# Kernel optimization log

Hardware: AMD Instinct MI355X
Metric: run time of the kernel (lower is better)

## Reference

```python
import jax, jax.numpy as jnp
import numpy as np

S, IN, H, D, B, BOT, IMG, TXT = 4, 4096, 2048, 6, 1024, 128, 768, 768


def _gelu(x):
    # torch nn.GELU default = exact erf gelu
    return jax.nn.gelu(x, approximate=False)


def _ln(x, g, b, eps=1e-5):
    mu = jnp.mean(x, axis=-1, keepdims=True)
    var = jnp.mean(jnp.square(x - mu), axis=-1, keepdims=True)
    return g * (x - mu) / jnp.sqrt(var + eps) + b


def setup_inputs() -> dict:
    key = jax.random.key(0)
    ks = jax.random.split(key, 16)
    n = lambda k, shp, s=0.02: jax.random.normal(k, shp, dtype=jnp.float32) * s
    return dict(
        voxels=jax.random.normal(ks[0], (B, IN), dtype=jnp.float32),
        subject_ids=jax.random.randint(ks[1], (B,), 0, S, dtype=jnp.int32),
        # per-subject encoder params, stacked on leading subject axis S
        ad_down_w=n(ks[2], (S, IN, BOT)), ad_down_b=n(ks[3], (S, BOT)),
        ad_up_w=n(ks[4], (S, BOT, IN)), ad_up_b=n(ks[5], (S, IN)),
        enc_w=n(ks[6], (S, IN, H)), enc_b=n(ks[7], (S, H)),
        enc_ln_g=jnp.ones((S, H), jnp.float32), enc_ln_b=jnp.zeros((S, H), jnp.float32),
        # shared ResidualStack params, stacked on leading depth axis D
        bb_w=n(ks[8], (D, H, H)), bb_b=n(ks[9], (D, H)),
        bb_ln_g=jnp.ones((D, H), jnp.float32), bb_ln_b=jnp.zeros((D, H), jnp.float32),
        # heads
        img_w=n(ks[10], (H, IMG)), img_b=n(ks[11], (IMG,)),
        txt_w=n(ks[12], (H, TXT)), txt_b=n(ks[13], (TXT,)),
    )


def _forward(voxels, subject_ids, ad_down_w, ad_down_b, ad_up_w, ad_up_b,
             enc_w, enc_b, enc_ln_g, enc_ln_b, bb_w, bb_b, bb_ln_g, bb_ln_b,
             img_w, img_b, txt_w, txt_b):
    # --- subject-routed encoders (dense dispatch over the small fixed subject set) ---
    def enc_one(dw, db, uw, ub, ew, eb, g, be):
        # BottleneckAdapter: x + up(gelu(down(x)))
        h = voxels + _gelu(voxels @ dw + db) @ uw + ub          # [B, IN]
        # Linear -> LayerNorm -> GELU (Dropout is identity in eval)
        return _gelu(_ln(h @ ew + eb, g, be))                    # [B, H]

    feats_all = jax.vmap(enc_one)(ad_down_w, ad_down_b, ad_up_w, ad_up_b,
                                  enc_w, enc_b, enc_ln_g, enc_ln_b)  # [S, B, H]
    x = feats_all[subject_ids, jnp.arange(voxels.shape[0])]          # [B, H] pick own subject

    # --- shared ResidualStack: x = x + gelu(ln(linear(x))) per block ---
    def step(x, p):
        w, b, g, be = p
        return x + _gelu(_ln(x @ w + b, g, be)), None

    x, _ = jax.lax.scan(step, x, (bb_w, bb_b, bb_ln_g, bb_ln_b))

    return x @ img_w + img_b, x @ txt_w + txt_b  # (image_embedding, text_embedding)


def reference(voxels, subject_ids, ad_down_w, ad_down_b, ad_up_w, ad_up_b,
              enc_w, enc_b, enc_ln_g, enc_ln_b, bb_w, bb_b, bb_ln_g, bb_ln_b,
              img_w, img_b, txt_w, txt_b):
    return _forward(voxels, subject_ids, ad_down_w, ad_down_b, ad_up_w, ad_up_b,
                    enc_w, enc_b, enc_ln_g, enc_ln_b, bb_w, bb_b, bb_ln_g, bb_ln_b,
                    img_w, img_b, txt_w, txt_b)
```

## Files before the change

kernel.cpp:

```cpp
#include <hip/hip_runtime.h>
#include <hip/hip_bf16.h>
#include <stdint.h>

typedef __bf16 bf16x8 __attribute__((ext_vector_type(8)));
typedef float  f32x4  __attribute__((ext_vector_type(4)));
typedef float  vf4    __attribute__((ext_vector_type(4)));

#define DEV __device__ __forceinline__

constexpr int SUBJ  = 4;
constexpr int IN    = 4096;
constexpr int H     = 2048;
constexpr int DEPTH = 6;
constexpr int BATCH = 1024;
constexpr int BOT   = 128;
constexpr int IMG   = 768;
constexpr int TXT   = 768;
constexpr int MP    = 1408;
constexpr int MT    = 11;

DEV float gelu_exact(float x){ return 0.5f*x*(1.0f + erff(x*0.70710678118654752440f)); }

DEV uint16_t bf16_bits(float x){
  __hip_bfloat16 h = __float2bfloat16(x);
  return *reinterpret_cast<uint16_t*>(&h);
}
DEV float bfu(uint32_t w, int hi){
  uint32_t x = hi ? (w & 0xffff0000u) : (w << 16);
  return __uint_as_float(x);
}
DEV float bf2f(uint16_t u){ uint32_t x = (uint32_t)u << 16; return __uint_as_float(x); }

struct CvtSeg { const float* src; size_t dst_off; };
struct CvtParams { CvtSeg s[6]; size_t total_items; };

__global__ void convert_weights(CvtParams p, __hip_bfloat16* __restrict__ dst){
  size_t it = (size_t)blockIdx.x*blockDim.x + threadIdx.x;
  if (it >= p.total_items) return;
  size_t e = it << 4;
  int si = 0;
  #pragma unroll
  for (int i = 1; i < 6; ++i) if (e >= p.s[i].dst_off) si = i;
  const float* s = p.s[si].src + (e - p.s[si].dst_off);
  float4 a = *reinterpret_cast<const float4*>(s);
  float4 b = *reinterpret_cast<const float4*>(s + 4);
  float4 c = *reinterpret_cast<const float4*>(s + 8);
  float4 d = *reinterpret_cast<const float4*>(s + 12);
  uint16_t o[16] = {bf16_bits(a.x), bf16_bits(a.y), bf16_bits(a.z), bf16_bits(a.w),
                    bf16_bits(b.x), bf16_bits(b.y), bf16_bits(b.z), bf16_bits(b.w),
                    bf16_bits(c.x), bf16_bits(c.y), bf16_bits(c.z), bf16_bits(c.w),
                    bf16_bits(d.x), bf16_bits(d.y), bf16_bits(d.z), bf16_bits(d.w)};
  *reinterpret_cast<uint4*>(dst + e)     = *reinterpret_cast<const uint4*>(&o[0]);
  *reinterpret_cast<uint4*>(dst + e + 8) = *reinterpret_cast<const uint4*>(&o[8]);
}

__global__ void sort_kernel(const int* __restrict__ ids, int* __restrict__ rowmap,
                            int* __restrict__ tileS){
  __shared__ int hist[16][4];
  __shared__ int basew[16][4];
  __shared__ int pstart[5];
  int tid = threadIdx.x;
  if (tid < MP) rowmap[tid] = -1;
  if (tid + 1024 < MP) rowmap[tid + 1024] = -1;
  int w = tid >> 6, lane = tid & 63;
  int my = ids[tid];
  unsigned long long mymask = 0ull;
  #pragma unroll
  for (int s = 0; s < 4; ++s){
    unsigned long long m = __ballot(my == s);
    if (lane == 0) hist[w][s] = (int)__popcll(m);
    if (s == my) mymask = m;
  }
  int myrank = (int)__popcll(mymask & ((1ull << lane) - 1ull));
  __syncthreads();
  if (tid == 0){
    for (int s = 0; s < 4; ++s){
      int run = 0;
      for (int ww = 0; ww < 16; ++ww){ basew[ww][s] = run; run += hist[ww][s]; }
      hist[0][s] = run;
    }
    pstart[0] = 0;
    for (int s = 0; s < 4; ++s) pstart[s+1] = pstart[s] + ((hist[0][s] + 127) & ~127);
  }
  __syncthreads();
  int pos = pstart[my] + basew[w][my] + myrank;
  rowmap[pos] = tid;
  if (tid < MT){
    int row0 = tid << 7, s = -1;
    for (int ss = 0; ss < 4; ++ss) if (row0 >= pstart[ss] && row0 < pstart[ss+1]) s = ss;
    tileS[tid] = s;
  }
}

__global__ void gather_voxels(const float* __restrict__ vox, const int* __restrict__ rowmap,
                              __hip_bfloat16* __restrict__ Vs){
  int r = blockIdx.x, tid = threadIdx.x;
  int orig = rowmap[r];
  #pragma unroll
  for (int i = 0; i < 4; ++i){
    int c = (i*256 + tid) << 2;
    float4 v = {0.f,0.f,0.f,0.f};
    if (orig >= 0) v = *reinterpret_cast<const float4*>(vox + (size_t)orig*IN + c);
    __hip_bfloat16 o[4] = {__float2bfloat16(v.x), __float2bfloat16(v.y),
                           __float2bfloat16(v.z), __float2bfloat16(v.w)};
    *reinterpret_cast<uint2*>(Vs + (size_t)r*IN + c) = *reinterpret_cast<const uint2*>(o);
  }
}

enum { EPI_SPLIT = 0, EPI_RES_BF16 = 1, EPI_HEADS = 3 };

template<int EPI, int TAG>
__global__ __launch_bounds__(256, 2)
void gemm_bf16(const __hip_bfloat16* __restrict__ A, int lda,
               const __hip_bfloat16* __restrict__ Bw, int ldn, long long wsub,
               const int* __restrict__ tileS, const int* __restrict__ rowmap,
               int nx, int qnt, int ksplit,
               const float* __restrict__ bias, int biassub,
               const float* __restrict__ resid, int ldres,
               __hip_bfloat16* __restrict__ outb, int ldo,
               size_t pstride, const __hip_bfloat16* __restrict__ Bw2)
{
  int b   = blockIdx.x;
  int xcd = b & 7;
  int r0  = b >> 3;
  int mt  = r0 % MT;
  int q   = r0 / MT;
  int kzi = xcd / nx + (q / qnt) * (8 / nx);
  int nt  = (q % qnt) * nx + (xcd % nx);

  int s = tileS[mt];
  if (s < 0) return;
  const __hip_bfloat16* Ab = A + (size_t)mt*128*lda;

  const __hip_bfloat16* Bb;
  int ntl = nt;
  if constexpr (EPI == EPI_HEADS){
    if (nt < 6){ Bb = Bw  + (size_t)nt*128; }
    else       { Bb = Bw2 + (size_t)(nt-6)*128; }
    ntl = nt;
  } else {
    Bb = Bw + (size_t)s*wsub + (size_t)nt*128;
  }

  int kb = kzi * ksplit;
  int nk = ksplit >> 6;

  __shared__ __hip_bfloat16 sA[2][128*64];
  __shared__ __hip_bfloat16 sB[2][128*64];

  int tid = threadIdx.x;
  int lane = tid & 63;
  int wv = tid >> 6, wr = wv >> 1, wc = wv & 1;

  int kq = tid >> 5;
  int nq = tid & 31;
  int n4 = nq << 2;

  f32x4 acc[4][4];
  #pragma unroll
  for (int i = 0; i < 4; ++i)
    #pragma unroll
    for (int j = 0; j < 4; ++j) acc[i][j] = (f32x4){0.f,0.f,0.f,0.f};

  auto stageA = [&](int buf, int k0){
    #pragma unroll
    for (int i = 0; i < 4; ++i){
      int cell = i*256 + tid;
      int row = cell >> 3, cc = cell & 7;
      int kg = k0 + ((cc ^ (row & 7)) << 3);
      __builtin_amdgcn_global_load_lds(
        (const __attribute__((address_space(1))) void*)(Ab + (size_t)row*lda + kg),
        (__attribute__((address_space(3))) void*)(&sA[buf][cell<<3]), 16, 0, 0);
    }
  };

  auto stageB_load = [&](int k0g, uint2* F){
    const __hip_bfloat16* p = Bb + (size_t)(k0g + (kq<<3))*ldn + n4;
    #pragma unroll
    for (int rr = 0; rr < 8; ++rr)
      F[rr] = *reinterpret_cast<const uint2*>(p + (size_t)rr*ldn);
  };
  auto stageB_write = [&](int buf, const uint2* F){
    #pragma unroll
    for (int j = 0; j < 4; ++j){
      int n = n4 + j;
      int cell = (kq ^ (n >> 3) ^ n) & 7;
      auto US = [&](int rr)->uint32_t{
        return (((const uint32_t*)&F[rr])[j >> 1] >> ((j & 1) * 16)) & 0xffffu;
      };
      uint4 d;
      d.x = US(0) | (US(1) << 16);
      d.y = US(2) | (US(3) << 16);
      d.z = US(4) | (US(5) << 16);
      d.w = US(6) | (US(7) << 16);
      *reinterpret_cast<uint4*>(&sB[buf][(n<<6) + (cell<<3)]) = d;
    }
  };

  uint2 F[8];
  stageB_load(kb, F);
  stageA(0, kb);
  stageB_write(0, F);
  __syncthreads();

  for (int t = 0; t < nk; ++t){
    if (t+1 < nk){
      stageB_load(kb + ((t+1)<<6), F);
      stageA((t+1)&1, kb + ((t+1)<<6));
    }
    const char* baseA = (const char*)(&sA[t&1][0]);
    const char* baseB = (const char*)(&sB[t&1][0]);
    int rA = (wr<<6) + (lane & 15);
    int rB = (wc<<6) + (lane & 15);
    #pragma unroll
    for (int kk = 0; kk < 2; ++kk){
      int koffA = ((((kk<<5) + ((lane>>4)<<3)) << 1)) ^ ((lane & 7) << 4);
      bf16x8 av[4], bv[4];
      #pragma unroll
      for (int f = 0; f < 4; ++f){
        int rowA = rA + f*16;
        av[f] = *reinterpret_cast<const bf16x8*>(baseA + (size_t)rowA*128 + koffA);
        int rowB = rB + f*16;
        int cellB = (((kk<<2) + (lane>>4)) ^ (rowB >> 3) ^ rowB) & 7;
        bv[f] = *reinterpret_cast<const bf16x8*>(baseB + (size_t)rowB*128 + (cellB<<4));
      }
      #pragma unroll
      for (int i = 0; i < 4; ++i)
        #pragma unroll
        for (int j = 0; j < 4; ++j)
          acc[i][j] = __builtin_amdgcn_mfma_f32_16x16x32_bf16(av[i], bv[j], acc[i][j], 0, 0, 0);
    }
    if (t+1 < nk) stageB_write((t+1)&1, F);
    __syncthreads();
  }

  #pragma unroll
  for (int i = 0; i < 4; ++i){
    int rbase = (mt<<7) + (wr<<6) + (i<<4) + ((lane>>4)<<2);
    #pragma unroll
    for (int j = 0; j < 4; ++j){
      int colp = (wc<<6) + (j<<4) + (lane & 15);
      #pragma unroll
      for (int qq = 0; qq < 4; ++qq){
        int r = rbase + qq;
        float v = acc[i][j][qq];
        if constexpr (EPI == EPI_SPLIT){
          int col = (nt<<7) + colp;
          outb[(size_t)kzi*pstride + (size_t)r*ldo + col] = __float2bfloat16(v);
        } else if constexpr (EPI == EPI_RES_BF16){
          int col = (nt<<7) + colp;
          int orig = rowmap[r];
          if (orig >= 0){
            v += bias[(size_t)s*biassub + col] + resid[(size_t)orig*ldres + col];
            outb[(size_t)r*ldo + col] = __float2bfloat16(v);
          }
        } else {
          int col = (ntl<<7) + colp;
          outb[(size_t)kzi*pstride + (size_t)r*ldo + col] = __float2bfloat16(v);
        }
      }
    }
  }
}

template<int NPART>
__global__ void t1_epilogue(const __hip_bfloat16* __restrict__ Tp, const float* __restrict__ db,
                            const int* __restrict__ rowmap, const int* __restrict__ tileS,
                            __hip_bfloat16* __restrict__ T1){
  int idx = blockIdx.x*256 + threadIdx.x;
  int r = idx >> 7, c = idx & 127;
  float v = 0.f;
  if (rowmap[r] >= 0){
    int s = tileS[r >> 7];
    float acc = 0.f;
    #pragma unroll
    for (int p = 0; p < NPART; ++p)
      acc += bf2f(*reinterpret_cast<const uint16_t*>(Tp + (size_t)p*MP*BOT + idx));
    v = gelu_exact(acc + db[s*BOT + c]);
  }
  T1[idx] = __float2bfloat16(v);
}

template<int RES, int NPART>
__global__ void ln_gelu_kernel(const __hip_bfloat16* __restrict__ Zp, size_t pstride,
                               const float* __restrict__ g,
                               const float* __restrict__ b, int gsub,
                               const float* __restrict__ lb,
                               const int* __restrict__ tileS, const int* __restrict__ rowmap,
                               __hip_bfloat16* __restrict__ Xb){
  int r = blockIdx.x, tid = threadIdx.x;
  size_t rowoff = (size_t)r * H;
  int c0 = tid << 3;
  int orig = rowmap[r];
  if (orig < 0){
    uint4 zu = {0u,0u,0u,0u};
    *reinterpret_cast<uint4*>(Xb + rowoff + c0) = zu;
    return;
  }
  int si = gsub ? tileS[r>>7] : 0;
  const float* gp  = g  + (size_t)si*gsub;
  const float* bp  = b  + (size_t)si*gsub;
  const float* lbp = lb + (size_t)si*gsub;
  float z[8];
  #pragma unroll
  for (int j = 0; j < 8; ++j) z[j] = lbp[c0+j];
  #pragma unroll
  for (int p = 0; p < NPART; ++p){
    uint4 v = *reinterpret_cast<const uint4*>(Zp + p*pstride + rowoff + c0);
    z[0] += bfu(v.x,0); z[1] += bfu(v.x,1);
    z[2] += bfu(v.y,0); z[3] += bfu(v.y,1);
    z[4] += bfu(v.z,0); z[5] += bfu(v.z,1);
    z[6] += bfu(v.w,0); z[7] += bfu(v.w,1);
  }
  float s1 = 0.f, s2 = 0.f;
  #pragma unroll
  for (int j = 0; j < 8; ++j){ s1 += z[j]; s2 += z[j]*z[j]; }
  #pragma unroll
  for (int m = 32; m >= 1; m >>= 1){ s1 += __shfl_xor(s1, m); s2 += __shfl_xor(s2, m); }
  __shared__ float red[4][2];
  int wv = tid >> 6, lane = tid & 63;
  if (lane == 0){ red[wv][0] = s1; red[wv][1] = s2; }
  __syncthreads();
  s1 = red[0][0]+red[1][0]+red[2][0]+red[3][0];
  s2 = red[0][1]+red[1][1]+red[2][1]+red[3][1];
  const float invH = 1.f / (float)H;
  float mu  = s1 * invH;
  float var = s2 * invH - mu*mu;
  float rs  = rsqrtf(var + 1e-5f);
  float o[8];
  #pragma unroll
  for (int j = 0; j < 8; ++j){
    float t = (z[j]-mu)*rs*gp[c0+j] + bp[c0+j];
    o[j] = gelu_exact(t);
  }
  if constexpr (RES){
    uint4 xv = *reinterpret_cast<const uint4*>(Xb + rowoff + c0);
    o[0] += bfu(xv.x,0); o[1] += bfu(xv.x,1);
    o[2] += bfu(xv.y,0); o[3] += bfu(xv.y,1);
    o[4] += bfu(xv.z,0); o[5] += bfu(xv.z,1);
    o[6] += bfu(xv.w,0); o[7] += bfu(xv.w,1);
  }
  __hip_bfloat16 ob[8];
  #pragma unroll
  for (int j = 0; j < 8; ++j) ob[j] = __float2bfloat16(o[j]);
  *reinterpret_cast<uint4*>(Xb + rowoff + c0) = *reinterpret_cast<const uint4*>(ob);
}

template<int NPART>
__global__ void head_combine(const __hip_bfloat16* __restrict__ Hp, size_t pstride,
                             const float* __restrict__ img_b, const float* __restrict__ txt_b,
                             const int* __restrict__ rowmap,
                             float* __restrict__ oimg, float* __restrict__ otxt){
  int r = blockIdx.x;
  int orig = rowmap[r];
  if (orig < 0) return;
  int col = threadIdx.x << 2;
  size_t base = (size_t)r*(IMG+TXT) + col;
  float4 acc = {0.f,0.f,0.f,0.f};
  #pragma unroll
  for (int p = 0; p < NPART; ++p){
    uint2 u = *reinterpret_cast<const uint2*>(Hp + (size_t)p*pstride + base);
    acc.x += bfu(u.x,0); acc.y += bfu(u.x,1);
    acc.z += bfu(u.y,0); acc.w += bfu(u.y,1);
  }
  float4 bb = (col < IMG)
            ? *reinterpret_cast<const float4*>(img_b + col)
            : *reinterpret_cast<const float4*>(txt_b + (col - IMG));
  float4 o = {acc.x+bb.x, acc.y+bb.y, acc.z+bb.z, acc.w+bb.w};
  if (col < IMG) *reinterpret_cast<float4*>(oimg + (size_t)orig*IMG + col) = o;
  else           *reinterpret_cast<float4*>(otxt + (size_t)orig*TXT + (col-IMG)) = o;
}

extern "C" void kernel_launch(void* const* d_in, const int* in_sizes, int n_in,
                              void* d_out, int out_size, void* d_ws, size_t ws_size,
                              hipStream_t stream){
  (void)in_sizes; (void)n_in; (void)out_size; (void)ws_size;
  const float* vox       = (const float*)d_in[0];
  const int*   ids       = (const int*)  d_in[1];
  const float* ad_down_w = (const float*)d_in[2];
  const float* ad_down_b = (const float*)d_in[3];
  const float* ad_up_w   = (const float*)d_in[4];
  const float* ad_up_b   = (const float*)d_in[5];
  const float* enc_w     = (const float*)d_in[6];
  const float* enc_b     = (const float*)d_in[7];
  const float* enc_ln_g  = (const float*)d_in[8];
  const float* enc_ln_bb = (const float*)d_in[9];
  const float* bb_w      = (const float*)d_in[10];
  const float* bb_b      = (const float*)d_in[11];
  const float* bb_ln_g   = (const float*)d_in[12];
  const float* bb_ln_b   = (const float*)d_in[13];
  const float* img_w     = (const float*)d_in[14];
  const float* img_b     = (const float*)d_in[15];
  const float* txt_w     = (const float*)d_in[16];
  const float* txt_b     = (const float*)d_in[17];
  float* out = (float*)d_out;

  const size_t N_DOWN = (size_t)SUBJ*IN*BOT;
  const size_t N_UP   = (size_t)SUBJ*BOT*IN;
  const size_t N_ENC  = (size_t)SUBJ*IN*H;
  const size_t N_BB   = (size_t)DEPTH*H*H;
  const size_t N_IMG  = (size_t)H*IMG;
  const size_t N_TXT  = (size_t)H*TXT;

  char* wp = (char*)d_ws;
  auto alloc = [&](size_t bytes)->char*{ char* p = wp; wp += (bytes + 255) & ~(size_t)255; return p; };
  int* rowmap = (int*)alloc(MP * sizeof(int));
  int* tileS  = (int*)alloc(MT * sizeof(int));
  __hip_bfloat16* Wbf = (__hip_bfloat16*)alloc((N_DOWN+N_UP+N_ENC+N_BB+N_IMG+N_TXT)*2);
  __hip_bfloat16* w_down = Wbf;
  __hip_bfloat16* w_up   = w_down + N_DOWN;
  __hip_bfloat16* w_enc  = w_up   + N_UP;
  __hip_bfloat16* w_bb   = w_enc  + N_ENC;
  __hip_bfloat16* w_img  = w_bb   + N_BB;
  __hip_bfloat16* w_txt  = w_img  + N_IMG;
  __hip_bfloat16* Vs    = (__hip_bfloat16*)alloc((size_t)MP*IN*2);
  __hip_bfloat16* T1p   = (__hip_bfloat16*)alloc((size_t)32*MP*BOT*2);
  __hip_bfloat16* T1    = (__hip_bfloat16*)alloc((size_t)MP*BOT*2);
  __hip_bfloat16* Hs    = (__hip_bfloat16*)alloc((size_t)MP*IN*2);
  __hip_bfloat16* Zp    = (__hip_bfloat16*)alloc((size_t)4*MP*H*2);
  __hip_bfloat16* Hp    = Zp;
  __hip_bfloat16* Xb    = (__hip_bfloat16*)alloc((size_t)MP*H*2);

  const size_t ZPS = (size_t)MP*H;
  const size_t TPS = (size_t)MP*BOT;
  const size_t HPS = (size_t)MP*(IMG+TXT);

  CvtParams cp;
  size_t off = 0;
  cp.s[0] = {ad_down_w, off}; off += N_DOWN;
  cp.s[1] = {ad_up_w,   off}; off += N_UP;
  cp.s[2] = {enc_w,     off}; off += N_ENC;
  cp.s[3] = {bb_w,      off}; off += N_BB;
  cp.s[4] = {img_w,     off}; off += N_IMG;
  cp.s[5] = {txt_w,     off}; off += N_TXT;
  cp.total_items = off >> 4;
  int cvt_blocks = (int)((cp.total_items + 255) / 256);
  convert_weights<<<cvt_blocks, 256, 0, stream>>>(cp, Wbf);

  sort_kernel<<<1, 1024, 0, stream>>>(ids, rowmap, tileS);
  gather_voxels<<<MP, 256, 0, stream>>>(vox, rowmap, Vs);

  gemm_bf16<EPI_SPLIT,1><<<MT*32, 256, 0, stream>>>(
      Vs, IN, w_down, BOT, (long long)IN*BOT, tileS, rowmap, 1, 1, 128,
      nullptr, 0, nullptr, 0, T1p, BOT, TPS, nullptr);
  t1_epilogue<32><<<MP*BOT/256, 256, 0, stream>>>(T1p, ad_down_b, rowmap, tileS, T1);

  gemm_bf16<EPI_RES_BF16,2><<<MT*32, 256, 0, stream>>>(
      T1, BOT, w_up, IN, (long long)BOT*IN, tileS, rowmap, 8, 4, 128,
      ad_up_b, IN, vox, IN, Hs, IN, 0, nullptr);

  gemm_bf16<EPI_SPLIT,3><<<MT*8*8, 256, 0, stream>>>(
      Hs, IN, w_enc, H, (long long)IN*H, tileS, rowmap, 2, 8, 1024,
      nullptr, 0, nullptr, 0, Zp, H, ZPS, nullptr);
  ln_gelu_kernel<0,4><<<MP, 256, 0, stream>>>(Zp, ZPS, enc_ln_g, enc_ln_bb, H, enc_b,
                                              tileS, rowmap, Xb);

  for (int d = 0; d < DEPTH; ++d){
    gemm_bf16<EPI_SPLIT,4><<<MT*4*8, 256, 0, stream>>>(
        Xb, H, w_bb + (size_t)d*H*H, H, 0, tileS, rowmap, 4, 4, 1024,
        nullptr, 0, nullptr, 0, Zp, H, ZPS, nullptr);
    ln_gelu_kernel<1,2><<<MP, 256, 0, stream>>>(Zp, ZPS, bb_ln_g + (size_t)d*H,
                                                bb_ln_b + (size_t)d*H, 0, bb_b + (size_t)d*H,
                                                tileS, rowmap, Xb);
  }

  gemm_bf16<EPI_HEADS,5><<<MT*3*8, 256, 0, stream>>>(
      Xb, H, w_img, IMG, 0, tileS, rowmap, 4, 3, 1024,
      nullptr, 0, nullptr, 0, Hp, IMG+TXT, HPS, w_txt);
  head_combine<2><<<MP, 384, 0, stream>>>(Hp, HPS, img_b, txt_b, rowmap,
                                          out, out + (size_t)BATCH*IMG);
}
```

Measured before the change: 433.4 us.

## Overlap weight bf16 conversion with preceding GEMMs via extra tail blocks

The single up-front weight conversion kernel is split up. Each weight tensor is now converted by extra blocks appended to the grid of the GEMM that runs just before that weight is first needed, so conversion overlaps with GEMM work. Only the adapter-down weights are still converted by a standalone kernel. This removes a serial memory-bound pass at the start. The cost is extra blocks competing with GEMM blocks for CUs and bandwidth, plus a larger kernel signature.

```diff
diff --git a/kernel.cpp b/kernel.cpp
--- a/kernel.cpp
+++ b/kernel.cpp
@@ -4,7 +4,6 @@
 
 typedef __bf16 bf16x8 __attribute__((ext_vector_type(8)));
 typedef float  f32x4  __attribute__((ext_vector_type(4)));
-typedef float  vf4    __attribute__((ext_vector_type(4)));
 
 #define DEV __device__ __forceinline__
 
@@ -31,27 +30,24 @@
 }
 DEV float bf2f(uint16_t u){ uint32_t x = (uint32_t)u << 16; return __uint_as_float(x); }
 
-struct CvtSeg { const float* src; size_t dst_off; };
-struct CvtParams { CvtSeg s[6]; size_t total_items; };
-
-__global__ void convert_weights(CvtParams p, __hip_bfloat16* __restrict__ dst){
-  size_t it = (size_t)blockIdx.x*blockDim.x + threadIdx.x;
-  if (it >= p.total_items) return;
-  size_t e = it << 4;
-  int si = 0;
-  #pragma unroll
-  for (int i = 1; i < 6; ++i) if (e >= p.s[i].dst_off) si = i;
-  const float* s = p.s[si].src + (e - p.s[si].dst_off);
+DEV void cvt16(const float* __restrict__ s, __hip_bfloat16* __restrict__ d){
   float4 a = *reinterpret_cast<const float4*>(s);
   float4 b = *reinterpret_cast<const float4*>(s + 4);
   float4 c = *reinterpret_cast<const float4*>(s + 8);
-  float4 d = *reinterpret_cast<const float4*>(s + 12);
+  float4 e = *reinterpret_cast<const float4*>(s + 12);
   uint16_t o[16] = {bf16_bits(a.x), bf16_bits(a.y), bf16_bits(a.z), bf16_bits(a.w),
                     bf16_bits(b.x), bf16_bits(b.y), bf16_bits(b.z), bf16_bits(b.w),
                     bf16_bits(c.x), bf16_bits(c.y), bf16_bits(c.z), bf16_bits(c.w),
-                    bf16_bits(d.x), bf16_bits(d.y), bf16_bits(d.z), bf16_bits(d.w)};
-  *reinterpret_cast<uint4*>(dst + e)     = *reinterpret_cast<const uint4*>(&o[0]);
-  *reinterpret_cast<uint4*>(dst + e + 8) = *reinterpret_cast<const uint4*>(&o[8]);
+                    bf16_bits(e.x), bf16_bits(e.y), bf16_bits(e.z), bf16_bits(e.w)};
+  *reinterpret_cast<uint4*>(d)     = *reinterpret_cast<const uint4*>(&o[0]);
+  *reinterpret_cast<uint4*>(d + 8) = *reinterpret_cast<const uint4*>(&o[8]);
+}
+
+__global__ void convert_plain(const float* __restrict__ src, __hip_bfloat16* __restrict__ dst,
+                              size_t items){
+  size_t it = (size_t)blockIdx.x*blockDim.x + threadIdx.x;
+  if (it >= items) return;
+  cvt16(src + (it<<4), dst + (it<<4));
 }
 
 __global__ void sort_kernel(const int* __restrict__ ids, int* __restrict__ rowmap,
@@ -118,9 +114,16 @@
                const float* __restrict__ bias, int biassub,
                const float* __restrict__ resid, int ldres,
                __hip_bfloat16* __restrict__ outb, int ldo,
-               size_t pstride, const __hip_bfloat16* __restrict__ Bw2)
+               size_t pstride, const __hip_bfloat16* __restrict__ Bw2,
+               int ggrid, const float* __restrict__ csrc,
+               __hip_bfloat16* __restrict__ cdst, size_t citems)
 {
-  int b   = blockIdx.x;
+  int b = blockIdx.x;
+  if (b >= ggrid){
+    size_t it = (size_t)(b - ggrid)*blockDim.x + threadIdx.x;
+    if (it < citems) cvt16(csrc + (it<<4), cdst + (it<<4));
+    return;
+  }
   int xcd = b & 7;
   int r0  = b >> 3;
   int mt  = r0 % MT;
@@ -425,40 +428,42 @@
   const size_t TPS = (size_t)MP*BOT;
   const size_t HPS = (size_t)MP*(IMG+TXT);
 
-  CvtParams cp;
-  size_t off = 0;
-  cp.s[0] = {ad_down_w, off}; off += N_DOWN;
-  cp.s[1] = {ad_up_w,   off}; off += N_UP;
-  cp.s[2] = {enc_w,     off}; off += N_ENC;
-  cp.s[3] = {bb_w,      off}; off += N_BB;
-  cp.s[4] = {img_w,     off}; off += N_IMG;
-  cp.s[5] = {txt_w,     off}; off += N_TXT;
-  cp.total_items = off >> 4;
-  int cvt_blocks = (int)((cp.total_items + 255) / 256);
-  convert_weights<<<cvt_blocks, 256, 0, stream>>>(cp, Wbf);
+  const size_t I_DOWN = N_DOWN >> 4, I_UP = N_UP >> 4, I_ENC = N_ENC >> 4;
+  const size_t I_BB = N_BB >> 4, I_IMG = N_IMG >> 4, I_TXT = N_TXT >> 4;
+  auto nb = [](size_t items){ return (int)((items + 255) / 256); };
+
+  convert_plain<<<nb(I_DOWN), 256, 0, stream>>>(ad_down_w, w_down, I_DOWN);
 
   sort_kernel<<<1, 1024, 0, stream>>>(ids, rowmap, tileS);
   gather_voxels<<<MP, 256, 0, stream>>>(vox, rowmap, Vs);
 
-  gemm_bf16<EPI_SPLIT,1><<<MT*32, 256, 0, stream>>>(
+  gemm_bf16<EPI_SPLIT,1><<<MT*32 + nb(I_UP), 256, 0, stream>>>(
       Vs, IN, w_down, BOT, (long long)IN*BOT, tileS, rowmap, 1, 1, 128,
-      nullptr, 0, nullptr, 0, T1p, BOT, TPS, nullptr);
+      nullptr, 0, nullptr, 0, T1p, BOT, TPS, nullptr,
+      MT*32, ad_up_w, w_up, I_UP);
   t1_epilogue<32><<<MP*BOT/256, 256, 0, stream>>>(T1p, ad_down_b, rowmap, tileS, T1);
 
-  gemm_bf16<EPI_RES_BF16,2><<<MT*32, 256, 0, stream>>>(
+  gemm_bf16<EPI_RES_BF16,2><<<MT*32 + nb(I_ENC), 256, 0, stream>>>(
       T1, BOT, w_up, IN, (long long)BOT*IN, tileS, rowmap, 8, 4, 128,
-      ad_up_b, IN, vox, IN, Hs, IN, 0, nullptr);
-
-  gemm_bf16<EPI_SPLIT,3><<<MT*8*8, 256, 0, stream>>>(
+      ad_up_b, IN, vox, IN, Hs, IN, 0, nullptr,
+      MT*32, enc_w, w_enc, I_ENC);
+
+  gemm_bf16<EPI_SPLIT,3><<<MT*8*8 + nb(I_BB), 256, 0, stream>>>(
       Hs, IN, w_enc, H, (long long)IN*H, tileS, rowmap, 2, 8, 1024,
-      nullptr, 0, nullptr, 0, Zp, H, ZPS, nullptr);
+      nullptr, 0, nullptr, 0, Zp, H, ZPS, nullptr,
+      MT*8*8, bb_w, w_bb, I_BB);
   ln_gelu_kernel<0,4><<<MP, 256, 0, stream>>>(Zp, ZPS, enc_ln_g, enc_ln_bb, H, enc_b,
                                               tileS, rowmap, Xb);
 
   for (int d = 0; d < DEPTH; ++d){
-    gemm_bf16<EPI_SPLIT,4><<<MT*4*8, 256, 0, stream>>>(
+    const float* cs = (d == 0) ? img_w : (d == 1) ? txt_w : nullptr;
+    __hip_bfloat16* cd = (d == 0) ? w_img : (d == 1) ? w_txt : nullptr;
+    size_t ci = (d == 0) ? I_IMG : (d == 1) ? I_TXT : 0;
+    int tail = (d <= 1) ? nb(ci) : 0;
+    gemm_bf16<EPI_SPLIT,4><<<MT*4*8 + tail, 256, 0, stream>>>(
         Xb, H, w_bb + (size_t)d*H*H, H, 0, tileS, rowmap, 4, 4, 1024,
-        nullptr, 0, nullptr, 0, Zp, H, ZPS, nullptr);
+        nullptr, 0, nullptr, 0, Zp, H, ZPS, nullptr,
+        MT*4*8, cs, cd, ci);
     ln_gelu_kernel<1,2><<<MP, 256, 0, stream>>>(Zp, ZPS, bb_ln_g + (size_t)d*H,
                                                 bb_ln_b + (size_t)d*H, 0, bb_b + (size_t)d*H,
                                                 tileS, rowmap, Xb);
@@ -466,7 +471,8 @@
 
   gemm_bf16<EPI_HEADS,5><<<MT*3*8, 256, 0, stream>>>(
       Xb, H, w_img, IMG, 0, tileS, rowmap, 4, 3, 1024,
-      nullptr, 0, nullptr, 0, Hp, IMG+TXT, HPS, w_txt);
+      nullptr, 0, nullptr, 0, Hp, IMG+TXT, HPS, w_txt,
+      MT*3*8, nullptr, nullptr, 0);
   head_combine<2><<<MP, 384, 0, stream>>>(Hp, HPS, img_b, txt_b, rowmap,
                                           out, out + (size_t)BATCH*IMG);
 }
```

Measured after the change: 402.3 us (median of 2 runs). -7.2%, faster.
